# Kernel optimization log

Measured on AMD Instinct MI355X. Metric: run time of the kernel, lower is better.

The kernel has to match this reference:

```python
import jax, jax.numpy as jnp
import numpy as np

DIM = 1024
HEADS = 16
HEAD_DIM = 64
ROT_DIM = HEAD_DIM // 2  # RotaryEmbedding(dim=head_dim//2): rotates first 32 dims only
B, T, H, W = 2, 32, 18, 32


def setup_inputs() -> dict:
    key = jax.random.key(0)
    k1, k2, k3 = jax.random.split(key, 3)
    x = jax.random.normal(k1, (B, T, H, W, DIM), dtype=jnp.float32)
    w_qkv = jax.random.normal(k2, (3 * HEADS * HEAD_DIM, DIM), dtype=jnp.float32) * 0.02
    w_out = jax.random.normal(k3, (DIM, HEADS * HEAD_DIM), dtype=jnp.float32) * 0.02
    b_out = jnp.zeros((DIM,), dtype=jnp.float32)
    return {"x": x, "w_qkv": w_qkv, "w_out": w_out, "b_out": b_out}


def _rope(t, pos):
    # t: [N, h, T, d]. lucidrains convention: interleaved pairs, rotate first ROT_DIM dims.
    freqs = 1.0 / (10000.0 ** (jnp.arange(0, ROT_DIM, 2, dtype=jnp.float32) / ROT_DIM))  # [ROT_DIM/2]
    ang = pos[:, None] * freqs[None, :]          # [T, ROT_DIM/2]
    ang = jnp.repeat(ang, 2, axis=-1)            # [T, ROT_DIM] (each freq repeated for its pair)
    cos, sin = jnp.cos(ang), jnp.sin(ang)
    x_rot, x_pass = t[..., :ROT_DIM], t[..., ROT_DIM:]
    xr = x_rot.reshape(x_rot.shape[:-1] + (ROT_DIM // 2, 2))
    rot = jnp.stack([-xr[..., 1], xr[..., 0]], axis=-1).reshape(x_rot.shape)  # rotate_half
    return jnp.concatenate([x_rot * cos + rot * sin, x_pass], axis=-1)


def reference(x, w_qkv, w_out, b_out):
    b, t, h, w, d = x.shape
    # fused QKV projection (bias=False)
    qkv = jnp.einsum('bthwd,ed->bthwe', x, w_qkv)
    q, k, v = jnp.split(qkv, 3, axis=-1)

    def to_heads(u):
        # 'B T H W (h d) -> (B H W) h T d'
        u = u.reshape(b, t, h, w, HEADS, HEAD_DIM)
        return u.transpose(0, 2, 3, 4, 1, 5).reshape(b * h * w, HEADS, t, HEAD_DIM)

    q, k, v = to_heads(q), to_heads(k), to_heads(v)
    pos = jnp.arange(t, dtype=jnp.float32)
    q = _rope(q, pos)
    k = _rope(k, pos)

    scale = HEAD_DIM ** -0.5
    scores = jnp.einsum('nhqd,nhkd->nhqk', q, k) * scale  # [BHW, h, T, T]
    causal = jnp.tril(jnp.ones((t, t), dtype=bool))
    scores = jnp.where(causal, scores, -jnp.inf)
    attn = jax.nn.softmax(scores, axis=-1)
    o = jnp.einsum('nhqk,nhkd->nhqd', attn, v)
    # '(B H W) h T d -> B T H W (h d)'
    o = o.reshape(b, h, w, HEADS, t, HEAD_DIM).transpose(0, 4, 1, 2, 3, 5)
    o = o.reshape(b, t, h, w, HEADS * HEAD_DIM)
    return o @ w_out.T + b_out
```

## Files before the change

kernel.cpp:

```cpp
#include <hip/hip_runtime.h>
#include <cstdint>
#include <cstddef>

typedef __bf16 bf16;
typedef __attribute__((ext_vector_type(8))) bf16  bf16x8;
typedef __attribute__((ext_vector_type(4))) bf16  bf16x4;
typedef __attribute__((ext_vector_type(4))) float f32x4;

#define B_SZ   2
#define T_SZ   32
#define H_SZ   18
#define W_SZ   32
#define DIM    1024
#define NHEAD  16
#define HDIM   64
#define E3     3072
#define M_TOT  36864
#define T_STRIDE 576
#define GK     1024
#define NKT    16

__global__ void taa_cvt_bf16(const float* __restrict__ s, bf16* __restrict__ d, int n4) {
    int i = blockIdx.x * 256 + threadIdx.x;
    if (i >= n4) return;
    float4 v = ((const float4*)s)[i];
    bf16x4 o;
    o.x = (bf16)v.x; o.y = (bf16)v.y; o.z = (bf16)v.z; o.w = (bf16)v.w;
    ((bf16x4*)d)[i] = o;
}

__device__ __forceinline__ void async_copy_16(const bf16* g, bf16* l) {
    __builtin_amdgcn_global_load_lds((__attribute__((address_space(1))) void*)g,
                                     (__attribute__((address_space(3))) void*)l,
                                     16, 0, 0);
}

#define MFMA16(a, b, c) __builtin_amdgcn_mfma_f32_16x16x32_bf16((a), (b), (c), 0, 0, 0)

template<bool OUT_BF16>
__global__ __launch_bounds__(512, 2)
void taa_gemm256(const bf16* __restrict__ A, const bf16* __restrict__ Bm,
                 void* __restrict__ Cout, const float* __restrict__ bias, int N) {
    __shared__ __align__(16) bf16 sA[2][2][8192];
    __shared__ __align__(16) bf16 sB[2][2][8192];

    const int tid  = threadIdx.x;
    const int lane = tid & 63;
    const int wv   = tid >> 6;
    const int wm   = wv >> 2;
    const int wn   = wv & 3;
    const int fr   = lane & 15;
    const int fq   = lane >> 4;

    const int ntn = N >> 8;
    const int nwg = gridDim.x;
    const int bid = blockIdx.x;
    const int swz = (bid & 7) * (nwg >> 3) + (bid >> 3);
    const int bm  = (swz / ntn) << 8;
    const int bn  = (swz % ntn) << 8;

    const int srow = tid >> 3;
    const int scol = ((tid & 7) ^ (srow & 7)) << 3;
    const bf16* gA0 = A  + (size_t)(bm + srow) * GK + scol;
    const bf16* gB0 = Bm + (size_t)(bn + srow) * GK + scol;

    const int swx = (fr & 7) << 4;
    const int cs0 = (fq * 16) ^ swx;
    const int cs1 = (64 + fq * 16) ^ swx;

    f32x4 acc[2][2][4][2];
#pragma unroll
    for (int ms = 0; ms < 2; ms++)
#pragma unroll
        for (int ns = 0; ns < 2; ns++)
#pragma unroll
            for (int i = 0; i < 4; i++)
#pragma unroll
                for (int j = 0; j < 2; j++)
                    acc[ms][ns][i][j] = (f32x4){0.f, 0.f, 0.f, 0.f};

    auto stage = [&](const bf16* g0, bf16* lbase, int h, int kt) {
        const bf16* g = g0 + (size_t)(h * 128) * GK + kt * 64;
        async_copy_16(g,                    lbase + h * 8192 + tid * 8);
        async_copy_16(g + (size_t)64 * GK,  lbase + h * 8192 + 4096 + tid * 8);
    };

    stage(gB0, &sB[0][0][0], 0, 0); stage(gB0, &sB[0][0][0], 1, 0);
    stage(gA0, &sA[0][0][0], 0, 0); stage(gA0, &sA[0][0][0], 1, 0);
    asm volatile("s_waitcnt vmcnt(0)" ::: "memory");
    __builtin_amdgcn_s_barrier();
    asm volatile("" ::: "memory");

#pragma unroll 2
    for (int kt = 0; kt < NKT; ++kt) {
        const int buf = kt & 1;
        const char* ab = (const char*)&sA[buf][wm][0] + fr * 128;
        const char* bb = (const char*)&sB[buf][wn >> 1][0] + ((wn & 1) * 64 + fr) * 128;

        if (kt + 1 < NKT) {
            stage(gB0, &sB[buf ^ 1][0][0], 0, kt + 1);
            stage(gB0, &sB[buf ^ 1][0][0], 1, kt + 1);
            stage(gA0, &sA[buf ^ 1][0][0], 0, kt + 1);
            stage(gA0, &sA[buf ^ 1][0][0], 1, kt + 1);
        }

        bf16x8 af[4][2];
        bf16x8 ag[4][2];
        bf16x8 bf0[2][2];
        bf16x8 bf1[2][2];

        af[0][0] = *(const bf16x8*)(ab + cs0);
        af[0][1] = *(const bf16x8*)(ab + cs1);
#pragma unroll
        for (int j = 0; j < 2; j++) {
            bf0[j][0] = *(const bf16x8*)(bb + j * 2048 + cs0);
            bf0[j][1] = *(const bf16x8*)(bb + j * 2048 + cs1);
        }
#pragma unroll
        for (int i = 1; i < 4; i++) {
            af[i][0] = *(const bf16x8*)(ab + i * 2048 + cs0);
            af[i][1] = *(const bf16x8*)(ab + i * 2048 + cs1);
        }
#pragma unroll
        for (int j = 0; j < 2; j++) {
            bf1[j][0] = *(const bf16x8*)(bb + 4096 + j * 2048 + cs0);
            bf1[j][1] = *(const bf16x8*)(bb + 4096 + j * 2048 + cs1);
        }
#pragma unroll
        for (int i = 0; i < 4; i++) {
            ag[i][0] = *(const bf16x8*)(ab + 8192 + i * 2048 + cs0);
            ag[i][1] = *(const bf16x8*)(ab + 8192 + i * 2048 + cs1);
        }

        __builtin_amdgcn_s_setprio(1);
#pragma unroll
        for (int i = 0; i < 4; i++)
#pragma unroll
            for (int j = 0; j < 2; j++) {
                acc[0][0][i][j] = MFMA16(af[i][0], bf0[j][0], acc[0][0][i][j]);
                acc[0][0][i][j] = MFMA16(af[i][1], bf0[j][1], acc[0][0][i][j]);
            }
#pragma unroll
        for (int i = 0; i < 4; i++)
#pragma unroll
            for (int j = 0; j < 2; j++) {
                acc[0][1][i][j] = MFMA16(af[i][0], bf1[j][0], acc[0][1][i][j]);
                acc[0][1][i][j] = MFMA16(af[i][1], bf1[j][1], acc[0][1][i][j]);
            }
#pragma unroll
        for (int i = 0; i < 4; i++)
#pragma unroll
            for (int j = 0; j < 2; j++) {
                acc[1][1][i][j] = MFMA16(ag[i][0], bf1[j][0], acc[1][1][i][j]);
                acc[1][1][i][j] = MFMA16(ag[i][1], bf1[j][1], acc[1][1][i][j]);
            }
#pragma unroll
        for (int i = 0; i < 4; i++)
#pragma unroll
            for (int j = 0; j < 2; j++) {
                acc[1][0][i][j] = MFMA16(ag[i][0], bf0[j][0], acc[1][0][i][j]);
                acc[1][0][i][j] = MFMA16(ag[i][1], bf0[j][1], acc[1][0][i][j]);
            }
        __builtin_amdgcn_s_setprio(0);

        asm volatile("s_waitcnt lgkmcnt(0) vmcnt(0)" ::: "memory");
        __builtin_amdgcn_s_barrier();
        asm volatile("" ::: "memory");
    }

    if constexpr (OUT_BF16) {
        bf16* C = (bf16*)Cout;
#pragma unroll
        for (int ms = 0; ms < 2; ms++)
#pragma unroll
            for (int ns = 0; ns < 2; ns++)
#pragma unroll
                for (int i = 0; i < 4; i++)
#pragma unroll
                    for (int j = 0; j < 2; j++)
#pragma unroll
                        for (int r = 0; r < 4; r++) {
                            const int row = bm + wm * 128 + ms * 64 + i * 16 + fq * 4 + r;
                            const int col = bn + wn * 64 + ns * 32 + j * 16 + fr;
                            C[(size_t)row * N + col] = (bf16)acc[ms][ns][i][j][r];
                        }
    } else {
        float* C = (float*)Cout;
#pragma unroll
        for (int ms = 0; ms < 2; ms++)
#pragma unroll
            for (int ns = 0; ns < 2; ns++)
#pragma unroll
                for (int i = 0; i < 4; i++)
#pragma unroll
                    for (int j = 0; j < 2; j++)
#pragma unroll
                        for (int r = 0; r < 4; r++) {
                            const int row = bm + wm * 128 + ms * 64 + i * 16 + fq * 4 + r;
                            const int col = bn + wn * 64 + ns * 32 + j * 16 + fr;
                            C[(size_t)row * N + col] = acc[ms][ns][i][j][r] + bias[col];
                        }
    }
}

__global__ __launch_bounds__(128)
void taa_attn_mfma(const bf16* __restrict__ qkv, bf16* __restrict__ o) {
    __shared__ __align__(16) bf16 sQ[32 * 72];
    __shared__ __align__(16) bf16 sK[32 * 72];
    __shared__ __align__(16) bf16 sVt[64 * 40];

    const int tid  = threadIdx.x;
    const int lane = tid & 63;
    const int wv   = tid >> 6;
    const int bid  = blockIdx.x;
    const int head = bid & 15;
    const int n    = bid >> 4;
    const int w_sp = n & 31;
    const int h_sp = (n >> 5) % 18;
    const int b    = n / (18 * 32);
    const int m0   = b * 18432 + h_sp * 32 + w_sp;

    {
        const int tl = tid >> 3;
        const int dl = (tid & 7) * 8;
#pragma unroll
        for (int it = 0; it < 2; ++it) {
            const int t = it * 16 + tl;
            const size_t rb = (size_t)(m0 + t * T_STRIDE) * E3 + head * 64 + dl;
            bf16x8 q8 = *(const bf16x8*)(qkv + rb);
            bf16x8 k8 = *(const bf16x8*)(qkv + rb + 1024);
            bf16x8 v8 = *(const bf16x8*)(qkv + rb + 2048);
            float qf[8], kf[8];
#pragma unroll
            for (int j = 0; j < 8; j++) { qf[j] = (float)q8[j]; kf[j] = (float)k8[j]; }
            if (dl < 32) {
#pragma unroll
                for (int p = 0; p < 4; p++) {
                    const int fi = dl / 2 + p;
                    float freq = exp2f(-(float)fi * 0.830482024f);
                    float ang  = (float)t * freq;
                    float s, c;
                    __sincosf(ang, &s, &c);
                    float a = qf[2 * p], bb = qf[2 * p + 1];
                    qf[2 * p]     = a * c - bb * s;
                    qf[2 * p + 1] = bb * c + a * s;
                    a = kf[2 * p]; bb = kf[2 * p + 1];
                    kf[2 * p]     = a * c - bb * s;
                    kf[2 * p + 1] = bb * c + a * s;
                }
            }
            bf16x8 qo, ko;
#pragma unroll
            for (int j = 0; j < 8; j++) { qo[j] = (bf16)qf[j]; ko[j] = (bf16)kf[j]; }
            *(bf16x8*)&sQ[t * 72 + dl] = qo;
            *(bf16x8*)&sK[t * 72 + dl] = ko;
#pragma unroll
            for (int j = 0; j < 8; j++) sVt[(dl + j) * 40 + t] = v8[j];
        }
    }
    __syncthreads();

    const int fr = lane & 15;
    const int fq = lane >> 4;
    const int mt = wv;

    f32x4 S[2];
    S[0] = (f32x4){0.f, 0.f, 0.f, 0.f};
    S[1] = (f32x4){0.f, 0.f, 0.f, 0.f};

    bf16x8 kb0[2], kb1[2];
#pragma unroll
    for (int nt = 0; nt < 2; nt++) {
        kb0[nt] = *(const bf16x8*)&sK[(nt * 16 + fr) * 72 + fq * 8];
        kb1[nt] = *(const bf16x8*)&sK[(nt * 16 + fr) * 72 + 32 + fq * 8];
    }
    {
        bf16x8 a0 = *(const bf16x8*)&sQ[(mt * 16 + fr) * 72 + fq * 8];
        bf16x8 a1 = *(const bf16x8*)&sQ[(mt * 16 + fr) * 72 + 32 + fq * 8];
#pragma unroll
        for (int nt = 0; nt < 2; nt++) {
            S[nt] = __builtin_amdgcn_mfma_f32_16x16x32_bf16(a0, kb0[nt], S[nt], 0, 0, 0);
            S[nt] = __builtin_amdgcn_mfma_f32_16x16x32_bf16(a1, kb1[nt], S[nt], 0, 0, 0);
        }
    }

    float P[2][4];
#pragma unroll
    for (int r = 0; r < 4; r++) {
        const int row = mt * 16 + fq * 4 + r;
        float s0 = S[0][r] * 0.125f;
        float s1 = S[1][r] * 0.125f;
        if (fr > row)      s0 = -1e30f;
        if (16 + fr > row) s1 = -1e30f;
        float mx = fmaxf(s0, s1);
#pragma unroll
        for (int mk = 1; mk <= 8; mk <<= 1) mx = fmaxf(mx, __shfl_xor(mx, mk, 64));
        float e0 = __expf(s0 - mx);
        float e1 = __expf(s1 - mx);
        float sm = e0 + e1;
#pragma unroll
        for (int mk = 1; mk <= 8; mk <<= 1) sm += __shfl_xor(sm, mk, 64);
        float inv = 1.0f / sm;
        P[0][r] = e0 * inv;
        P[1][r] = e1 * inv;
    }

    __syncthreads();
    bf16* const sP = sQ;

#pragma unroll
    for (int nt = 0; nt < 2; nt++)
#pragma unroll
        for (int r = 0; r < 4; r++)
            sP[(mt * 16 + fq * 4 + r) * 40 + nt * 16 + fr] = (bf16)P[nt][r];

    f32x4 O[4];
#pragma unroll
    for (int dt = 0; dt < 4; dt++) O[dt] = (f32x4){0.f, 0.f, 0.f, 0.f};
    {
        bf16x8 a = *(const bf16x8*)&sP[(mt * 16 + fr) * 40 + fq * 8];
#pragma unroll
        for (int dt = 0; dt < 4; dt++) {
            bf16x8 bvv = *(const bf16x8*)&sVt[(dt * 16 + fr) * 40 + fq * 8];
            O[dt] = __builtin_amdgcn_mfma_f32_16x16x32_bf16(a, bvv, O[dt], 0, 0, 0);
        }
    }

#pragma unroll
    for (int dt = 0; dt < 4; dt++)
#pragma unroll
        for (int r = 0; r < 4; r++) {
            const int t = mt * 16 + fq * 4 + r;
            const int d = dt * 16 + fr;
            o[(size_t)(m0 + t * T_STRIDE) * DIM + head * 64 + d] = (bf16)O[dt][r];
        }
}

extern "C" void kernel_launch(void* const* d_in, const int* in_sizes, int n_in,
                              void* d_out, int out_size, void* d_ws, size_t ws_size,
                              hipStream_t stream) {
    const float* x     = (const float*)d_in[0];
    const float* w_qkv = (const float*)d_in[1];
    const float* w_out = (const float*)d_in[2];
    const float* b_out = (const float*)d_in[3];

    char* ws = (char*)d_ws;
    bf16* x_b    = (bf16*)(ws + 0);
    bf16* wqkv_b = (bf16*)(ws + 75497472);
    bf16* wout_b = (bf16*)(ws + 81788928);
    bf16* qkv_b  = (bf16*)(ws + 83886080);
    bf16* o_b    = (bf16*)(ws + 310378496);

    taa_cvt_bf16<<<(M_TOT * DIM / 4 + 255) / 256, 256, 0, stream>>>(x, x_b, M_TOT * DIM / 4);
    taa_cvt_bf16<<<(E3 * DIM / 4 + 255) / 256, 256, 0, stream>>>(w_qkv, wqkv_b, E3 * DIM / 4);
    taa_cvt_bf16<<<(DIM * DIM / 4 + 255) / 256, 256, 0, stream>>>(w_out, wout_b, DIM * DIM / 4);

    taa_gemm256<true><<<dim3((M_TOT / 256) * (E3 / 256)), 512, 0, stream>>>(
        x_b, wqkv_b, (void*)qkv_b, nullptr, E3);

    taa_attn_mfma<<<1152 * 16, 128, 0, stream>>>(qkv_b, o_b);

    taa_gemm256<false><<<dim3((M_TOT / 256) * (DIM / 256)), 512, 0, stream>>>(
        o_b, wout_b, d_out, b_out, DIM);
}
```

Before: 695.1 us.

## Write QKV in head-major panels and attention output sequence-contiguous for coalesced access

The QKV GEMM epilogue now scatters its output into per-head panels laid out as [section*16+head][spatial][t][d], so each attention block reads its Q/K/V as contiguous 4KB chunks instead of 32 strided rows. The attention kernel stages its output through LDS and writes 16-byte vectors in an (n, t) ordered layout, and the output GEMM's epilogue remaps rows back to the original (b, t, h, w) order. This targets the scattered, poorly coalesced global reads and writes in the attention kernel. The cost is scattered 2-byte stores in the QKV GEMM epilogue and extra index arithmetic, which may hurt write coalescing there.

```diff
diff --git a/kernel.cpp b/kernel.cpp
--- a/kernel.cpp
+++ b/kernel.cpp
@@ -16,9 +16,11 @@
 #define HDIM   64
 #define E3     3072
 #define M_TOT  36864
-#define T_STRIDE 576
+#define N_SP   1152
 #define GK     1024
 #define NKT    16
+#define HPANEL 2359296
+
 
 __global__ void taa_cvt_bf16(const float* __restrict__ s, bf16* __restrict__ d, int n4) {
     int i = blockIdx.x * 256 + threadIdx.x;
@@ -170,36 +172,48 @@
 
     if constexpr (OUT_BF16) {
         bf16* C = (bf16*)Cout;
+        const int sh = (bn + wn * 64) >> 6;
+        bf16* Cw = C + (size_t)sh * HPANEL;
 #pragma unroll
         for (int ms = 0; ms < 2; ms++)
 #pragma unroll
-            for (int ns = 0; ns < 2; ns++)
-#pragma unroll
-                for (int i = 0; i < 4; i++)
-#pragma unroll
-                    for (int j = 0; j < 2; j++)
-#pragma unroll
-                        for (int r = 0; r < 4; r++) {
-                            const int row = bm + wm * 128 + ms * 64 + i * 16 + fq * 4 + r;
-                            const int col = bn + wn * 64 + ns * 32 + j * 16 + fr;
-                            C[(size_t)row * N + col] = (bf16)acc[ms][ns][i][j][r];
-                        }
+            for (int i = 0; i < 4; i++)
+#pragma unroll
+                for (int r = 0; r < 4; r++) {
+                    const int m   = bm + wm * 128 + ms * 64 + i * 16 + fq * 4 + r;
+                    const int b   = m / 18432;
+                    const int rem = m - b * 18432;
+                    const int t   = rem / 576;
+                    const int sp  = rem - t * 576;
+                    const size_t ro = (size_t)(b * 576 + sp) * 2048 + t * 64 + fr;
+#pragma unroll
+                    for (int ns = 0; ns < 2; ns++)
+#pragma unroll
+                        for (int j = 0; j < 2; j++)
+                            Cw[ro + ns * 32 + j * 16] = (bf16)acc[ms][ns][i][j][r];
+                }
     } else {
         float* C = (float*)Cout;
 #pragma unroll
         for (int ms = 0; ms < 2; ms++)
 #pragma unroll
-            for (int ns = 0; ns < 2; ns++)
-#pragma unroll
-                for (int i = 0; i < 4; i++)
-#pragma unroll
-                    for (int j = 0; j < 2; j++)
-#pragma unroll
-                        for (int r = 0; r < 4; r++) {
-                            const int row = bm + wm * 128 + ms * 64 + i * 16 + fq * 4 + r;
+            for (int i = 0; i < 4; i++)
+#pragma unroll
+                for (int r = 0; r < 4; r++) {
+                    const int mp = bm + wm * 128 + ms * 64 + i * 16 + fq * 4 + r;
+                    const int nn = mp >> 5;
+                    const int t  = mp & 31;
+                    const int b  = nn / 576;
+                    const int sp = nn - b * 576;
+                    const size_t mo = (size_t)b * 18432 + (size_t)t * 576 + sp;
+#pragma unroll
+                    for (int ns = 0; ns < 2; ns++)
+#pragma unroll
+                        for (int j = 0; j < 2; j++) {
                             const int col = bn + wn * 64 + ns * 32 + j * 16 + fr;
-                            C[(size_t)row * N + col] = acc[ms][ns][i][j][r] + bias[col];
+                            C[mo * DIM + col] = acc[ms][ns][i][j][r] + bias[col];
                         }
+                }
     }
 }
 
@@ -215,47 +229,56 @@
     const int bid  = blockIdx.x;
     const int head = bid & 15;
     const int n    = bid >> 4;
-    const int w_sp = n & 31;
-    const int h_sp = (n >> 5) % 18;
-    const int b    = n / (18 * 32);
-    const int m0   = b * 18432 + h_sp * 32 + w_sp;
+
+    const bf16* qb = qkv + ((size_t)head        * N_SP + n) * 2048;
+    const bf16* kb = qkv + ((size_t)(16 + head) * N_SP + n) * 2048;
+    const bf16* vb = qkv + ((size_t)(32 + head) * N_SP + n) * 2048;
 
     {
-        const int tl = tid >> 3;
-        const int dl = (tid & 7) * 8;
-#pragma unroll
-        for (int it = 0; it < 2; ++it) {
-            const int t = it * 16 + tl;
-            const size_t rb = (size_t)(m0 + t * T_STRIDE) * E3 + head * 64 + dl;
-            bf16x8 q8 = *(const bf16x8*)(qkv + rb);
-            bf16x8 k8 = *(const bf16x8*)(qkv + rb + 1024);
-            bf16x8 v8 = *(const bf16x8*)(qkv + rb + 2048);
-            float qf[8], kf[8];
-#pragma unroll
-            for (int j = 0; j < 8; j++) { qf[j] = (float)q8[j]; kf[j] = (float)k8[j]; }
-            if (dl < 32) {
-#pragma unroll
-                for (int p = 0; p < 4; p++) {
-                    const int fi = dl / 2 + p;
-                    float freq = exp2f(-(float)fi * 0.830482024f);
-                    float ang  = (float)t * freq;
-                    float s, c;
-                    __sincosf(ang, &s, &c);
-                    float a = qf[2 * p], bb = qf[2 * p + 1];
-                    qf[2 * p]     = a * c - bb * s;
-                    qf[2 * p + 1] = bb * c + a * s;
-                    a = kf[2 * p]; bb = kf[2 * p + 1];
-                    kf[2 * p]     = a * c - bb * s;
-                    kf[2 * p + 1] = bb * c + a * s;
-                }
-            }
-            bf16x8 qo, ko;
-#pragma unroll
-            for (int j = 0; j < 8; j++) { qo[j] = (bf16)qf[j]; ko[j] = (bf16)kf[j]; }
-            *(bf16x8*)&sQ[t * 72 + dl] = qo;
-            *(bf16x8*)&sK[t * 72 + dl] = ko;
-#pragma unroll
-            for (int j = 0; j < 8; j++) sVt[(dl + j) * 40 + t] = v8[j];
+        const int t  = tid >> 2;
+        const int d0 = (tid & 3) << 4;
+        const int off = t * 64 + d0;
+        bf16x8 q8a = *(const bf16x8*)(qb + off);
+        bf16x8 q8b = *(const bf16x8*)(qb + off + 8);
+        bf16x8 k8a = *(const bf16x8*)(kb + off);
+        bf16x8 k8b = *(const bf16x8*)(kb + off + 8);
+        bf16x8 v8a = *(const bf16x8*)(vb + off);
+        bf16x8 v8b = *(const bf16x8*)(vb + off + 8);
+        if (d0 < 32) {
+            float qf[16], kf[16];
+#pragma unroll
+            for (int j = 0; j < 8; j++) {
+                qf[j] = (float)q8a[j]; qf[8 + j] = (float)q8b[j];
+                kf[j] = (float)k8a[j]; kf[8 + j] = (float)k8b[j];
+            }
+#pragma unroll
+            for (int p = 0; p < 8; p++) {
+                const int fi = (d0 >> 1) + p;
+                float freq = exp2f(-(float)fi * 0.830482024f);
+                float ang  = (float)t * freq;
+                float s, c;
+                __sincosf(ang, &s, &c);
+                float a = qf[2 * p], bb2 = qf[2 * p + 1];
+                qf[2 * p]     = a * c - bb2 * s;
+                qf[2 * p + 1] = bb2 * c + a * s;
+                a = kf[2 * p]; bb2 = kf[2 * p + 1];
+                kf[2 * p]     = a * c - bb2 * s;
+                kf[2 * p + 1] = bb2 * c + a * s;
+            }
+#pragma unroll
+            for (int j = 0; j < 8; j++) {
+                q8a[j] = (bf16)qf[j]; q8b[j] = (bf16)qf[8 + j];
+                k8a[j] = (bf16)kf[j]; k8b[j] = (bf16)kf[8 + j];
+            }
+        }
+        *(bf16x8*)&sQ[t * 72 + d0]     = q8a;
+        *(bf16x8*)&sQ[t * 72 + d0 + 8] = q8b;
+        *(bf16x8*)&sK[t * 72 + d0]     = k8a;
+        *(bf16x8*)&sK[t * 72 + d0 + 8] = k8b;
+#pragma unroll
+        for (int j = 0; j < 8; j++) {
+            sVt[(d0 + j) * 40 + t]     = v8a[j];
+            sVt[(d0 + 8 + j) * 40 + t] = v8b[j];
         }
     }
     __syncthreads();
@@ -329,11 +352,16 @@
 #pragma unroll
     for (int dt = 0; dt < 4; dt++)
 #pragma unroll
-        for (int r = 0; r < 4; r++) {
-            const int t = mt * 16 + fq * 4 + r;
-            const int d = dt * 16 + fr;
-            o[(size_t)(m0 + t * T_STRIDE) * DIM + head * 64 + d] = (bf16)O[dt][r];
-        }
+        for (int r = 0; r < 4; r++)
+            sK[(mt * 16 + fq * 4 + r) * 72 + dt * 16 + fr] = (bf16)O[dt][r];
+
+    const int tr = mt * 16 + (lane >> 2);
+    const int c0 = (lane & 3) << 4;
+    bf16x8 o0 = *(const bf16x8*)&sK[tr * 72 + c0];
+    bf16x8 o1 = *(const bf16x8*)&sK[tr * 72 + c0 + 8];
+    bf16* ob = o + ((size_t)n * 32 + tr) * DIM + head * 64 + c0;
+    *(bf16x8*)(ob)     = o0;
+    *(bf16x8*)(ob + 8) = o1;
 }
 
 extern "C" void kernel_launch(void* const* d_in, const int* in_sizes, int n_in,
@@ -358,7 +386,7 @@
     taa_gemm256<true><<<dim3((M_TOT / 256) * (E3 / 256)), 512, 0, stream>>>(
         x_b, wqkv_b, (void*)qkv_b, nullptr, E3);
 
-    taa_attn_mfma<<<1152 * 16, 128, 0, stream>>>(qkv_b, o_b);
+    taa_attn_mfma<<<N_SP * NHEAD, 128, 0, stream>>>(qkv_b, o_b);
 
     taa_gemm256<false><<<dim3((M_TOT / 256) * (DIM / 256)), 512, 0, stream>>>(
         o_b, wout_b, d_out, b_out, DIM);
```

After: 674.0 us. -3.0%, faster.
